# Kernel tuning notes

Hardware: AMD Instinct MI355X
Metric: run time of the kernel (lower is better)

Reference implementation:

```python
import jax, jax.numpy as jnp
import numpy as np

TYPE_NUM = 4
NUM_INPUTS = 128
BATCH = 4096
NODE_NUM = 256
HID = 16


def _xavier_uniform(key, shape, gain=1.414):
    fan_in, fan_out = shape[-2], shape[-1]
    lim = gain * (6.0 / (fan_in + fan_out)) ** 0.5
    return jax.random.uniform(key, shape, jnp.float32, -lim, lim)


def setup_inputs() -> dict:
    key = jax.random.key(0)
    k0, k1, k2, k3, k4 = jax.random.split(key, 5)
    x = jax.random.normal(k0, (BATCH, NODE_NUM, NUM_INPUTS), jnp.float32)
    a1 = _xavier_uniform(k1, (TYPE_NUM, 2 * NUM_INPUTS, HID))
    a2 = _xavier_uniform(k2, (TYPE_NUM, HID, 1))
    # binary neighbor mask over nodes; ensure at least one neighbor
    adj_mask = jax.random.randint(k3, (NODE_NUM,), 0, 2).astype(jnp.float32).at[0].set(1.0)
    type_index = jax.random.randint(k4, (BATCH,), 0, TYPE_NUM)
    node_index = 0
    return dict(x=x, a1=a1, a2=a2, adj_mask=adj_mask,
                node_index=node_index, type_index=type_index)


def reference(x, a1, a2, adj_mask, node_index, type_index):
    # x: [B, N, F]; a1: [T, 2F, H]; a2: [T, H, 1]; adj_mask: [N]; type_index: [B]
    B, N, Fdim = x.shape
    T = a1.shape[0]
    tgt = jnp.broadcast_to(x[:, node_index, :][:, None, :], (B, N, Fdim))
    concat = jnp.concatenate([tgt, x], axis=-1)            # [B, N, 2F]
    h = jax.nn.leaky_relu(jnp.einsum('bnc,tch->tbnh', concat, a1))   # [T, B, N, H]
    e = jax.nn.leaky_relu(jnp.einsum('tbnh,th->tbn', h, a2[:, :, 0]))  # [T, B, N]
    neg = jnp.asarray(-9e15, e.dtype)
    att = jnp.where(adj_mask > 0, e, neg)                  # mask broadcasts over [T,B,N]
    att = jax.nn.softmax(att, axis=-1) * adj_mask          # [T, B, N]
    onehot = jax.nn.one_hot(type_index, T, dtype=x.dtype)  # [B, T]
    probs = jnp.einsum('tbn,bt->bn', att, onehot)          # [B, N] -> Categorical probs
    return probs
```

## Files before the change

### kernel.cpp

```cpp
#include <hip/hip_runtime.h>
#include <math.h>

#define BATCH 4096
#define NODES 256
#define FDIM  128
#define HID   16

typedef __attribute__((ext_vector_type(8))) short short8;
typedef __attribute__((ext_vector_type(4))) float f32x4;

__device__ __forceinline__ short bf_trunc(float x) {
    return (short)(__float_as_uint(x) >> 16);
}
__device__ __forceinline__ float bf_back(short s) {
    return __uint_as_float(((unsigned)(unsigned short)s) << 16);
}
__device__ __forceinline__ void split8(float4 v0, float4 v1,
                                       short8& hi, short8& lo) {
    float v[8] = {v0.x, v0.y, v0.z, v0.w, v1.x, v1.y, v1.z, v1.w};
    #pragma unroll
    for (int j = 0; j < 8; ++j) {
        const short h = bf_trunc(v[j]);
        hi[j] = h;
        lo[j] = bf_trunc(v[j] - bf_back(h));
    }
}

__launch_bounds__(256, 2)
__global__ void mta_kernel(const float* __restrict__ x,
                           const float* __restrict__ a1,
                           const float* __restrict__ a2,
                           const float* __restrict__ adj,
                           const int*  __restrict__ node_index,
                           const int*  __restrict__ type_index,
                           float* __restrict__ out) {
    const int b    = blockIdx.x;
    const int tid  = threadIdx.x;
    const int lane = tid & 63;
    const int w    = tid >> 6;
    const int n    = lane & 15;
    const int g    = lane >> 4;

    __shared__ float es[NODES];
    __shared__ float part[16][17];
    __shared__ float c0s[HID];
    __shared__ float redm[4], reds[4];

    const int t  = __builtin_amdgcn_readfirstlane(type_index[b]);
    const int ni = __builtin_amdgcn_readfirstlane(node_index[0]);

    const float* At  = a1 + (size_t)t * (2 * FDIM * HID);
    const float* Ab  = At + FDIM * HID;
    const float* a2t = a2 + t * HID;
    const float* xb  = x + (size_t)b * NODES * FDIM;

    {
        const float* x0 = xb + (size_t)ni * FDIM;
        const int f2 = tid >> 4;
        const int h  = tid & 15;
        float p = 0.f;
        #pragma unroll
        for (int j = 0; j < 8; ++j) {
            const int f = f2 * 8 + j;
            p = fmaf(x0[f], At[f * HID + h], p);
        }
        part[f2][h] = p;
    }
    __syncthreads();
    if (tid < 16) {
        float s = 0.f;
        #pragma unroll
        for (int gg = 0; gg < 16; ++gg) s += part[gg][tid];
        c0s[tid] = s;
    }
    __syncthreads();

    short8 whi[4], wlo[4];
    #pragma unroll
    for (int kt = 0; kt < 4; ++kt) {
        float wv[8];
        #pragma unroll
        for (int j = 0; j < 8; ++j)
            wv[j] = Ab[(kt * 32 + g * 8 + j) * HID + n];
        float4 w0 = {wv[0], wv[1], wv[2], wv[3]};
        float4 w1 = {wv[4], wv[5], wv[6], wv[7]};
        split8(w0, w1, whi[kt], wlo[kt]);
    }

    const int rowbase = w * 64;
    f32x4 acc[4];
    #pragma unroll
    for (int mt = 0; mt < 4; ++mt) acc[mt] = (f32x4){0.f, 0.f, 0.f, 0.f};

    #pragma unroll
    for (int kt = 0; kt < 4; ++kt) {
        float4 ra[4][2];
        #pragma unroll
        for (int mt = 0; mt < 4; ++mt) {
            const float* p = xb + (size_t)(rowbase + mt * 16 + n) * FDIM
                           + kt * 32 + g * 8;
            ra[mt][0] = *(const float4*)p;
            ra[mt][1] = *(const float4*)(p + 4);
        }
        #pragma unroll
        for (int mt = 0; mt < 4; ++mt) {
            short8 ahi, alo;
            split8(ra[mt][0], ra[mt][1], ahi, alo);
            acc[mt] = __builtin_amdgcn_mfma_f32_16x16x32_bf16(ahi, whi[kt], acc[mt], 0, 0, 0);
            acc[mt] = __builtin_amdgcn_mfma_f32_16x16x32_bf16(ahi, wlo[kt], acc[mt], 0, 0, 0);
            acc[mt] = __builtin_amdgcn_mfma_f32_16x16x32_bf16(alo, whi[kt], acc[mt], 0, 0, 0);
        }
    }

    const float c0h = c0s[n];
    const float a2h = a2t[n];
    #pragma unroll
    for (int mt = 0; mt < 4; ++mt) {
        #pragma unroll
        for (int r = 0; r < 4; ++r) {
            float v = acc[mt][r] + c0h;
            v = (v > 0.f) ? v : 0.01f * v;
            float s = v * a2h;
            s += __shfl_xor(s, 1);
            s += __shfl_xor(s, 2);
            s += __shfl_xor(s, 4);
            s += __shfl_xor(s, 8);
            float e = (s > 0.f) ? s : 0.01f * s;
            if (n == 0) es[rowbase + mt * 16 + g * 4 + r] = e;
        }
    }
    __syncthreads();

    const float ee  = es[tid];
    const float m   = adj[tid];
    float       val = (m > 0.f) ? ee : -INFINITY;

    float mx = val;
    #pragma unroll
    for (int off = 32; off; off >>= 1) mx = fmaxf(mx, __shfl_xor(mx, off));
    const int wid = tid >> 6;
    if ((tid & 63) == 0) redm[wid] = mx;
    __syncthreads();
    mx = fmaxf(fmaxf(redm[0], redm[1]), fmaxf(redm[2], redm[3]));

    float pr = (m > 0.f) ? __expf(ee - mx) : 0.f;
    float s = pr;
    #pragma unroll
    for (int off = 32; off; off >>= 1) s += __shfl_xor(s, off);
    if ((tid & 63) == 0) reds[wid] = s;
    __syncthreads();
    const float Z = reds[0] + reds[1] + reds[2] + reds[3];

    out[(size_t)b * NODES + tid] = pr / Z;
}

extern "C" void kernel_launch(void* const* d_in, const int* in_sizes, int n_in,
                              void* d_out, int out_size, void* d_ws, size_t ws_size,
                              hipStream_t stream) {
    const float* x   = (const float*)d_in[0];
    const float* a1  = (const float*)d_in[1];
    const float* a2  = (const float*)d_in[2];
    const float* adj = (const float*)d_in[3];
    const int*   ni  = (const int*)d_in[4];
    const int*   ti  = (const int*)d_in[5];
    float* out = (float*)d_out;

    mta_kernel<<<BATCH, NODES, 0, stream>>>(x, a1, a2, adj, ni, ti, out);
}
```

Baseline: 101.5 us.

## Drop weight low-part MFMA, round-to-nearest bf16 split, raise occupancy

Weights are now rounded to a single bf16 (round-to-nearest) instead of a hi/lo split, so each tile needs two MFMAs instead of three. The activation hi/lo split also switches from truncation to round-to-nearest. Launch bounds go up to three blocks per SM, and loads are issued in groups of two row tiles rather than four to lower register pressure. This cuts MFMA work and aims for more occupancy, but weight precision drops to bf16 and there is less memory-level parallelism per wave.

```diff
diff --git a/kernel.cpp b/kernel.cpp
--- a/kernel.cpp
+++ b/kernel.cpp
@@ -9,8 +9,9 @@
 typedef __attribute__((ext_vector_type(8))) short short8;
 typedef __attribute__((ext_vector_type(4))) float f32x4;
 
-__device__ __forceinline__ short bf_trunc(float x) {
-    return (short)(__float_as_uint(x) >> 16);
+__device__ __forceinline__ short bf_rn(float x) {
+    const unsigned u = __float_as_uint(x);
+    return (short)((u + 0x7FFF + ((u >> 16) & 1)) >> 16);
 }
 __device__ __forceinline__ float bf_back(short s) {
     return __uint_as_float(((unsigned)(unsigned short)s) << 16);
@@ -20,13 +21,13 @@
     float v[8] = {v0.x, v0.y, v0.z, v0.w, v1.x, v1.y, v1.z, v1.w};
     #pragma unroll
     for (int j = 0; j < 8; ++j) {
-        const short h = bf_trunc(v[j]);
+        const short h = bf_rn(v[j]);
         hi[j] = h;
-        lo[j] = bf_trunc(v[j] - bf_back(h));
+        lo[j] = bf_rn(v[j] - bf_back(h));
     }
 }
 
-__launch_bounds__(256, 2)
+__launch_bounds__(256, 3)
 __global__ void mta_kernel(const float* __restrict__ x,
                            const float* __restrict__ a1,
                            const float* __restrict__ a2,
@@ -75,16 +76,12 @@
     }
     __syncthreads();
 
-    short8 whi[4], wlo[4];
+    short8 whi[4];
     #pragma unroll
     for (int kt = 0; kt < 4; ++kt) {
-        float wv[8];
         #pragma unroll
         for (int j = 0; j < 8; ++j)
-            wv[j] = Ab[(kt * 32 + g * 8 + j) * HID + n];
-        float4 w0 = {wv[0], wv[1], wv[2], wv[3]};
-        float4 w1 = {wv[4], wv[5], wv[6], wv[7]};
-        split8(w0, w1, whi[kt], wlo[kt]);
+            whi[kt][j] = bf_rn(Ab[(kt * 32 + g * 8 + j) * HID + n]);
     }
 
     const int rowbase = w * 64;
@@ -94,21 +91,26 @@
 
     #pragma unroll
     for (int kt = 0; kt < 4; ++kt) {
-        float4 ra[4][2];
         #pragma unroll
-        for (int mt = 0; mt < 4; ++mt) {
-            const float* p = xb + (size_t)(rowbase + mt * 16 + n) * FDIM
-                           + kt * 32 + g * 8;
-            ra[mt][0] = *(const float4*)p;
-            ra[mt][1] = *(const float4*)(p + 4);
-        }
-        #pragma unroll
-        for (int mt = 0; mt < 4; ++mt) {
-            short8 ahi, alo;
-            split8(ra[mt][0], ra[mt][1], ahi, alo);
-            acc[mt] = __builtin_amdgcn_mfma_f32_16x16x32_bf16(ahi, whi[kt], acc[mt], 0, 0, 0);
-            acc[mt] = __builtin_amdgcn_mfma_f32_16x16x32_bf16(ahi, wlo[kt], acc[mt], 0, 0, 0);
-            acc[mt] = __builtin_amdgcn_mfma_f32_16x16x32_bf16(alo, whi[kt], acc[mt], 0, 0, 0);
+        for (int mh = 0; mh < 4; mh += 2) {
+            float4 ra[2][2];
+            #pragma unroll
+            for (int i = 0; i < 2; ++i) {
+                const float* p = xb
+                    + (size_t)(rowbase + (mh + i) * 16 + n) * FDIM
+                    + kt * 32 + g * 8;
+                ra[i][0] = *(const float4*)p;
+                ra[i][1] = *(const float4*)(p + 4);
+            }
+            #pragma unroll
+            for (int i = 0; i < 2; ++i) {
+                short8 ahi, alo;
+                split8(ra[i][0], ra[i][1], ahi, alo);
+                acc[mh + i] = __builtin_amdgcn_mfma_f32_16x16x32_bf16(
+                    ahi, whi[kt], acc[mh + i], 0, 0, 0);
+                acc[mh + i] = __builtin_amdgcn_mfma_f32_16x16x32_bf16(
+                    alo, whi[kt], acc[mh + i], 0, 0, 0);
+            }
         }
     }
 
```

Result: slower. 105.4 us (+3.8%).
